# Kernel optimization log

Hardware: AMD Instinct MI355X
Metric: run time of the kernel (lower is better)

## Reference

```python
import jax, jax.numpy as jnp
import numpy as np

GN_EPS = 1e-5
NN_EPS = 1e-8


def _three_nn_interpolate(xyz1, xyz2, points2):
    # xyz1: (B,N,3), xyz2: (B,M,3), points2: (B,M,C) -> (B,N,C)
    src_sq = jnp.sum(xyz1 ** 2, axis=-1, keepdims=True)          # (B,N,1)
    dst_sq = jnp.sum(xyz2 ** 2, axis=-1)[:, None, :]             # (B,1,M)
    inner = jnp.einsum('bnd,bmd->bnm', xyz1, xyz2)               # (B,N,M)
    dist = src_sq - 2.0 * inner + dst_sq                         # (B,N,M)
    neg_d, idx = jax.lax.top_k(-dist, 3)                         # (B,N,3)
    d = -neg_d
    inv = 1.0 / (d + NN_EPS)
    w = inv / jnp.sum(inv, axis=-1, keepdims=True)               # (B,N,3)
    grouped = jax.vmap(lambda p, i: p[i])(points2, idx)          # (B,N,3,C)
    return jnp.sum(grouped * w[..., None], axis=2)               # (B,N,C)


def _group_norm(x, weight, bias, groups):
    # x: (B,C,N)
    B, C, N = x.shape
    xg = x.reshape(B, groups, C // groups, N)
    mu = jnp.mean(xg, axis=(2, 3), keepdims=True)
    var = jnp.var(xg, axis=(2, 3), keepdims=True)
    xg = (xg - mu) * jax.lax.rsqrt(var + GN_EPS)
    x = xg.reshape(B, C, N)
    return x * weight[None, :, None] + bias[None, :, None]


def setup_inputs() -> dict:
    key = jax.random.key(0)
    ks = jax.random.split(key, 10)
    B, N, M, C1, C2 = 8, 8192, 2048, 128, 256
    mlp = [256, 128]
    in_ch = C1 + C2
    inp = {
        'xyz1': jax.random.normal(ks[0], (B, N, 3), dtype=jnp.float32),
        'xyz2': jax.random.normal(ks[1], (B, M, 3), dtype=jnp.float32),
        'points1': jax.random.normal(ks[2], (B, N, C1), dtype=jnp.float32),
        'points2': jax.random.normal(ks[3], (B, M, C2), dtype=jnp.float32),
        'w0': jax.random.normal(ks[4], (mlp[0], in_ch), dtype=jnp.float32) * (1.0 / np.sqrt(in_ch)),
        'w1': jax.random.normal(ks[5], (mlp[1], mlp[0]), dtype=jnp.float32) * (1.0 / np.sqrt(mlp[0])),
        'gn0_w': jnp.ones((mlp[0],), dtype=jnp.float32),
        'gn0_b': jnp.zeros((mlp[0],), dtype=jnp.float32),
        'gn1_w': jnp.ones((mlp[1],), dtype=jnp.float32),
        'gn1_b': jnp.zeros((mlp[1],), dtype=jnp.float32),
    }
    return inp


def reference(xyz1, xyz2, points1, points2, w0, w1, gn0_w, gn0_b, gn1_w, gn1_b):
    interpolated = _three_nn_interpolate(xyz1, xyz2, points2)    # (B,N,C2)
    feat = jnp.concatenate([points1, interpolated], axis=-1)     # (B,N,C1+C2)
    # conv1d kernel size 1 == pointwise matmul; work in (B,C,N) layout for GN
    h = jnp.einsum('bnc,oc->bon', feat, w0)                      # (B,256,N)
    h = jax.nn.relu(_group_norm(h, gn0_w, gn0_b, groups=min(32, w0.shape[0])))
    h = jnp.einsum('bcn,oc->bon', h, w1)                         # (B,128,N)
    h = jax.nn.relu(_group_norm(h, gn1_w, gn1_b, groups=min(32, w1.shape[0])))
    return jnp.transpose(h, (0, 2, 1))                           # (B,N,128)
```

## Files before the change

kernel.cpp:

```cpp
#include <hip/hip_runtime.h>


#define DEVI __device__ __forceinline__

static constexpr int B  = 8;
static constexpr int N  = 8192;
static constexpr int M  = 2048;
static constexpr int C1 = 128;
static constexpr int C2 = 256;
static constexpr int CIN = C1 + C2;
static constexpr int H0 = 256;
static constexpr int H1 = 128;
static constexpr int BN = B * N;
static constexpr int NSEG = 8;
static constexpr int SEGL = M / NSEG;

typedef __bf16 bf16x8 __attribute__((ext_vector_type(8)));
typedef float  f32x4  __attribute__((ext_vector_type(4)));
typedef unsigned short ushort8v __attribute__((ext_vector_type(8)));

DEVI float bf2f(unsigned short u) {
    union { unsigned int i; float f; } v; v.i = ((unsigned int)u) << 16; return v.f;
}
DEVI unsigned short f2bf(float f) {
    union { float f; unsigned int i; } v; v.f = f;
    unsigned int x = v.i;
    return (unsigned short)((x + 0x7fffu + ((x >> 16) & 1u)) >> 16);
}
DEVI float ldin(const void* p, size_t i, int bf) {
    return bf ? bf2f(((const unsigned short*)p)[i]) : ((const float*)p)[i];
}
DEVI void ld8(const void* p, size_t i, int bf, float r[8]) {
    if (bf) {
        const ushort8v u = *(const ushort8v*)((const unsigned short*)p + i);
#pragma unroll
        for (int k = 0; k < 8; k++) r[k] = bf2f(u[k]);
    } else {
        const float4 a = *(const float4*)((const float*)p + i);
        const float4 b = *(const float4*)((const float*)p + i + 4);
        r[0] = a.x; r[1] = a.y; r[2] = a.z; r[3] = a.w;
        r[4] = b.x; r[5] = b.y; r[6] = b.z; r[7] = b.w;
    }
}
DEVI void ld8b(const unsigned short* p, size_t i, float r[8]) {
    const ushort8v u = *(const ushort8v*)(p + i);
#pragma unroll
    for (int k = 0; k < 8; k++) r[k] = bf2f(u[k]);
}

DEVI void gload16(const void* g, void* l) {
    __builtin_amdgcn_global_load_lds(
        (const __attribute__((address_space(1))) void*)g,
        (__attribute__((address_space(3))) void*)l, 16, 0, 0);
}

__global__ __launch_bounds__(64) void detect_dtype_kernel(const void* __restrict__ xyz1,
                                                          int* __restrict__ flag)
{
    const unsigned short* u = (const unsigned short*)xyz1;
    const int lane = threadIdx.x;
    const float av = fabsf(bf2f(u[2 * lane]));
    const bool in_range = (av >= 1e-4f && av <= 100.0f);
    const unsigned long long m = __ballot(in_range);
    if (lane == 0) flag[0] = (__popcll(m) >= 32) ? 1 : 0;
}

DEVI void cvt8(const void* src, unsigned short* dst, size_t j8, int bf) {
    if (bf) {
        *(ushort8v*)(dst + j8 * 8) = *(const ushort8v*)((const unsigned short*)src + j8 * 8);
    } else {
        float r[8];
        ld8(src, j8 * 8, 0, r);
        ushort8v o;
#pragma unroll
        for (int k = 0; k < 8; k++) o[k] = f2bf(r[k]);
        *(ushort8v*)(dst + j8 * 8) = o;
    }
}

__global__ __launch_bounds__(256) void prep_kernel(
    const void* __restrict__ w0, const void* __restrict__ w1,
    const void* __restrict__ p2, const void* __restrict__ xyz2,
    unsigned short* __restrict__ w0b, unsigned short* __restrict__ w1b,
    unsigned short* __restrict__ pb2,
    float4* __restrict__ c4, float* __restrict__ partz,
    const int* __restrict__ flag)
{
    const int bf = flag[0];
    constexpr int R0 = H0 * CIN / 8;
    constexpr int R1 = H1 * H0 / 8;
    constexpr int R2 = B * M;
    constexpr int R4 = B * M * C2 / 8;
    constexpr int R5 = 1024;
    constexpr int TOT = R0 + R1 + R2 + R4 + R5;
    for (int i = blockIdx.x * blockDim.x + threadIdx.x; i < TOT; i += gridDim.x * blockDim.x) {
        int j = i;
        if (j < R0) { cvt8(w0, w0b, j, bf); continue; }
        j -= R0;
        if (j < R1) { cvt8(w1, w1b, j, bf); continue; }
        j -= R1;
        if (j < R2) {
            const float x = ldin(xyz2, (size_t)j * 3 + 0, bf);
            const float y = ldin(xyz2, (size_t)j * 3 + 1, bf);
            const float z = ldin(xyz2, (size_t)j * 3 + 2, bf);
            const float sq = __fadd_rn(__fadd_rn(__fmul_rn(x, x), __fmul_rn(y, y)), __fmul_rn(z, z));
            c4[j] = make_float4(x, y, z, 0.5f * sq);
            continue;
        }
        j -= R2;
        if (j < R4) { cvt8(p2, pb2, j, bf); continue; }
        j -= R4;
        partz[j] = 0.f;
    }
}

__global__ __launch_bounds__(256) void knn3_split_kernel(
    const void* __restrict__ xyz1, const float4* __restrict__ c4,
    int* __restrict__ ci, const int* __restrict__ flag)
{
    const int bf = flag[0];
    const int tid = threadIdx.x;
    const int gid = blockIdx.x * 256 + tid;
    const int s = blockIdx.y;
    const int b = __builtin_amdgcn_readfirstlane(gid >> 13);

    const float x1 = ldin(xyz1, (size_t)gid * 3 + 0, bf);
    const float y1 = ldin(xyz1, (size_t)gid * 3 + 1, bf);
    const float z1 = ldin(xyz1, (size_t)gid * 3 + 2, bf);

    const float4* __restrict__ cand = c4 + b * M + s * SEGL;
    const int jbase = s * SEGL;
    constexpr int HALF = SEGL / 2;

    float a0 = 3.4e38f, a1 = 3.4e38f, a2 = 3.4e38f;
    int   ia0 = 0, ia1 = 0, ia2 = 0;
    float g0 = 3.4e38f, g1 = 3.4e38f, g2 = 3.4e38f;
    int   ig0 = 0, ig1 = 0, ig2 = 0;

#pragma unroll 4
    for (int j = 0; j < HALF; ++j) {
        const float4 pA = cand[j];
        const float4 pB = cand[j + HALF];
        const float sA = __builtin_fmaf(-x1, pA.x,
                          __builtin_fmaf(-y1, pA.y,
                           __builtin_fmaf(-z1, pA.z, pA.w)));
        const float sB = __builtin_fmaf(-x1, pB.x,
                          __builtin_fmaf(-y1, pB.y,
                           __builtin_fmaf(-z1, pB.z, pB.w)));
        {
            const int jn = jbase + j;
            const bool c0 = sA < a0;
            const float t1 = fmaxf(sA, a0); a0 = fminf(sA, a0);
            const int  tj1 = c0 ? ia0 : jn; ia0 = c0 ? jn : ia0;
            const bool c1 = t1 < a1;
            const float t2 = fmaxf(t1, a1); a1 = fminf(t1, a1);
            const int  tj2 = c1 ? ia1 : tj1; ia1 = c1 ? tj1 : ia1;
            const bool c2 = t2 < a2;
            a2 = fminf(t2, a2); ia2 = c2 ? tj2 : ia2;
        }
        {
            const int jn = jbase + HALF + j;
            const bool c0 = sB < g0;
            const float t1 = fmaxf(sB, g0); g0 = fminf(sB, g0);
            const int  tj1 = c0 ? ig0 : jn; ig0 = c0 ? jn : ig0;
            const bool c1 = t1 < g1;
            const float t2 = fmaxf(t1, g1); g1 = fminf(t1, g1);
            const int  tj2 = c1 ? ig1 : tj1; ig1 = c1 ? tj1 : ig1;
            const bool c2 = t2 < g2;
            g2 = fminf(t2, g2); ig2 = c2 ? tj2 : ig2;
        }
    }

    float mv[3] = { g0, g1, g2 };
    int   mi[3] = { ig0, ig1, ig2 };
#pragma unroll
    for (int k = 0; k < 3; ++k) {
        const float sv = mv[k]; const int jn = mi[k];
        const bool c0 = sv < a0;
        const float t1 = fmaxf(sv, a0); a0 = fminf(sv, a0);
        const int  tj1 = c0 ? ia0 : jn; ia0 = c0 ? jn : ia0;
        const bool c1 = t1 < a1;
        const float t2 = fmaxf(t1, a1); a1 = fminf(t1, a1);
        const int  tj2 = c1 ? ia1 : tj1; ia1 = c1 ? tj1 : ia1;
        const bool c2 = t2 < a2;
        a2 = fminf(t2, a2); ia2 = c2 ? tj2 : ia2;
    }

    ci[(size_t)(s * 3 + 0) * BN + gid] = ia0;
    ci[(size_t)(s * 3 + 1) * BN + gid] = ia1;
    ci[(size_t)(s * 3 + 2) * BN + gid] = ia2;
}

__global__ __launch_bounds__(256) void interp_merge_kernel(
    const void* __restrict__ p1, const unsigned short* __restrict__ pb2,
    const void* __restrict__ xyz1, const float4* __restrict__ c4,
    const int* __restrict__ ci,
    unsigned short* __restrict__ feat, const int* __restrict__ flag)
{
    __shared__ int   sidx[128][3];
    __shared__ float sw[128][3];

    const int bf = flag[0];
    const int t = threadIdx.x;
    const int qbase = blockIdx.x * 128;
    const int b = qbase >> 13;

    if (t < 128) {
        const int q = qbase + t;
        const float x1 = ldin(xyz1, (size_t)q * 3 + 0, bf);
        const float y1 = ldin(xyz1, (size_t)q * 3 + 1, bf);
        const float z1 = ldin(xyz1, (size_t)q * 3 + 2, bf);
        const float sq1 = __fadd_rn(__fadd_rn(__fmul_rn(x1, x1), __fmul_rn(y1, y1)), __fmul_rn(z1, z1));

        float bd0 = 3.4e38f, bd1 = 3.4e38f, bd2 = 3.4e38f;
        int   bi0 = 0x7fffffff, bi1 = 0x7fffffff, bi2 = 0x7fffffff;

#pragma unroll
        for (int k = 0; k < 3 * NSEG; ++k) {
            const int ix = ci[(size_t)k * BN + q];
            const float4 p = c4[b * M + ix];
            const float inner = __fadd_rn(__fadd_rn(__fmul_rn(x1, p.x), __fmul_rn(y1, p.y)),
                                          __fmul_rn(z1, p.z));
            const float pw2 = p.w + p.w;
            const float d = __fadd_rn(__fsub_rn(sq1, __fmul_rn(2.0f, inner)), pw2);
            const bool lt2 = (d < bd2) || (d == bd2 && ix < bi2);
            if (lt2) {
                const bool lt0 = (d < bd0) || (d == bd0 && ix < bi0);
                const bool lt1 = (d < bd1) || (d == bd1 && ix < bi1);
                if (lt0)      { bd2 = bd1; bi2 = bi1; bd1 = bd0; bi1 = bi0; bd0 = d; bi0 = ix; }
                else if (lt1) { bd2 = bd1; bi2 = bi1; bd1 = d; bi1 = ix; }
                else          { bd2 = d; bi2 = ix; }
            }
        }

        const float v0 = 1.0f / (bd0 + 1e-8f);
        const float v1 = 1.0f / (bd1 + 1e-8f);
        const float v2 = 1.0f / (bd2 + 1e-8f);
        const float s = v0 + v1 + v2;
        sidx[t][0] = bi0; sidx[t][1] = bi1; sidx[t][2] = bi2;
        sw[t][0] = v0 / s; sw[t][1] = v1 / s; sw[t][2] = v2 / s;
    }
    __syncthreads();

#pragma unroll 1
    for (int it = 0; it < 24; ++it) {
        const int tt = it * 256 + t;
        const int ql = tt / 48;
        const int c8 = tt % 48;
        const int c  = c8 * 8;
        const int q  = qbase + ql;
        ushort8v o;
        if (c < C1) {
            if (bf) {
                o = *(const ushort8v*)((const unsigned short*)p1 + (size_t)q * C1 + c);
            } else {
                float r[8];
                ld8(p1, (size_t)q * C1 + c, 0, r);
#pragma unroll
                for (int k = 0; k < 8; k++) o[k] = f2bf(r[k]);
            }
        } else {
            const int c2 = c - C1;
            float t0[8], t1[8], t2[8];
            ld8b(pb2, (size_t)(b * M + sidx[ql][0]) * C2 + c2, t0);
            ld8b(pb2, (size_t)(b * M + sidx[ql][1]) * C2 + c2, t1);
            ld8b(pb2, (size_t)(b * M + sidx[ql][2]) * C2 + c2, t2);
            const float w0v = sw[ql][0], w1v = sw[ql][1], w2v = sw[ql][2];
#pragma unroll
            for (int k = 0; k < 8; k++)
                o[k] = f2bf(w0v * t0[k] + w1v * t1[k] + w2v * t2[k]);
        }
        *(ushort8v*)(feat + (size_t)q * CIN + c) = o;
    }
}

__global__ __launch_bounds__(512) void gemm1_kernel(
    const unsigned short* __restrict__ A,
    const unsigned short* __restrict__ W,
    unsigned short* __restrict__ h0, float2* __restrict__ part)
{
    constexpr int K = CIN;
    constexpr int COUT = H0;
    __shared__ __align__(16) char lds[49152];

    const int tid = threadIdx.x;
    const int l   = tid & 63;
    const int w   = tid >> 6;
    const int rowBase = blockIdx.x * 128;
    const int b = rowBase >> 13;

    const int srow  = l >> 3;
    const int sslot = l & 7;

    f32x4 acc[4][4];
#pragma unroll
    for (int i = 0; i < 4; i++)
#pragma unroll
        for (int j = 0; j < 4; j++) acc[i][j] = (f32x4)0.0f;

    const int wr  = w >> 2;
    const int wc  = w & 3;
    const int rl  = l & 15;
    const int kq  = l >> 4;
    const int swz = (l & 7) << 4;
    int aoff[4], boff[4];
#pragma unroll
    for (int i = 0; i < 4; i++) {
        aoff[i] = (wr * 64 + i * 16 + rl) * 128;
        boff[i] = 16384 + (wc * 64 + i * 16 + rl) * 128;
    }

    constexpr int NT = K / 64;

#pragma unroll 1
    for (int t = 0; t < NT; ++t) {
        const int k0 = t * 64;
#pragma unroll
        for (int i = 0; i < 6; ++i) {
            const int ch = w * 6 + i;
            if (ch < 16) {
                const int r  = ch * 8 + srow;
                const int ke = (sslot ^ (r & 7)) << 3;
                gload16(A + ((size_t)(rowBase + r) * K + k0 + ke), lds + ch * 1024);
            } else {
                const int rb = (ch - 16) * 8 + srow;
                const int ke = (sslot ^ (rb & 7)) << 3;
                gload16(W + ((size_t)rb * K + k0 + ke), lds + 16384 + (ch - 16) * 1024);
            }
        }
        __syncthreads();
#pragma unroll
        for (int ks = 0; ks < 2; ++ks) {
            const int kb = (ks * 64 + kq * 16) ^ swz;
            bf16x8 af[4], bfr[4];
#pragma unroll
            for (int i = 0; i < 4; i++) af[i]  = *(const bf16x8*)(lds + aoff[i] + kb);
#pragma unroll
            for (int j = 0; j < 4; j++) bfr[j] = *(const bf16x8*)(lds + boff[j] + kb);
#pragma unroll
            for (int i = 0; i < 4; i++)
#pragma unroll
                for (int j = 0; j < 4; j++)
                    acc[i][j] = __builtin_amdgcn_mfma_f32_16x16x32_bf16(af[i], bfr[j], acc[i][j], 0, 0, 0);
        }
        __syncthreads();
    }

    const int crow = rowBase + wr * 64 + kq * 4;
    const int ccol = wc * 64 + rl;
    float gsum[4], gss[4];
#pragma unroll
    for (int j = 0; j < 4; j++) {
        float s = 0.f, ss = 0.f;
#pragma unroll
        for (int i = 0; i < 4; i++)
#pragma unroll
            for (int r = 0; r < 4; r++) {
                const unsigned short hb = f2bf(acc[i][j][r]);
                h0[(size_t)(crow + i * 16 + r) * COUT + ccol + j * 16] = hb;
                const float x = bf2f(hb);
                s += x; ss += x * x;
            }
        gsum[j] = s; gss[j] = ss;
    }
    __syncthreads();
    float2* sred = (float2*)lds;
    if (tid < 32) sred[tid] = make_float2(0.f, 0.f);
    __syncthreads();
#pragma unroll
    for (int j = 0; j < 4; j++) {
        const int g = wc * 8 + j * 2 + (rl >> 3);
        atomicAdd(&sred[g].x, gsum[j]);
        atomicAdd(&sred[g].y, gss[j]);
    }
    __syncthreads();
    if (tid < 32) {
        atomicAdd(&part[b * 32 + tid].x, sred[tid].x);
        atomicAdd(&part[b * 32 + tid].y, sred[tid].y);
    }
}

__global__ __launch_bounds__(256) void gemm2_kernel(
    const unsigned short* __restrict__ h0, const float2* __restrict__ part0,
    const void* __restrict__ gw, const void* __restrict__ gb,
    const unsigned short* __restrict__ W,
    unsigned short* __restrict__ h1, float2* __restrict__ part1,
    const int* __restrict__ flag)
{
    constexpr int K = H0;
    constexpr int COUT = H1;
    __shared__ __align__(16) char lds[32768];
    __shared__ float2 stlds[32];

    const int bf = flag[0];
    const int tid = threadIdx.x;
    const int l   = tid & 63;
    const int w   = tid >> 6;
    const int rowBase = blockIdx.x * 128;
    const int b = rowBase >> 13;

    if (tid < 32) {
        const float2 p = part0[b * 32 + tid];
        const float cnt = (float)N * 8.0f;
        const float mu  = p.x / cnt;
        const float var = p.y / cnt - mu * mu;
        stlds[tid] = make_float2(mu, rsqrtf(var + 1e-5f));
    }
    __syncthreads();

    const int srow  = l >> 3;
    const int sslot = l & 7;

    f32x4 acc[4][4];
#pragma unroll
    for (int i = 0; i < 4; i++)
#pragma unroll
        for (int j = 0; j < 4; j++) acc[i][j] = (f32x4)0.0f;

    const int wr  = (tid >> 7) & 1;
    const int wc  = (tid >> 6) & 1;
    const int rl  = l & 15;
    const int kq  = l >> 4;
    const int swz = (l & 7) << 4;
    int aoff[4], boff[4];
#pragma unroll
    for (int i = 0; i < 4; i++) {
        aoff[i] = (wr * 64 + i * 16 + rl) * 128;
        boff[i] = 16384 + (wc * 64 + i * 16 + rl) * 128;
    }

    constexpr int NT = K / 64;

#pragma unroll 1
    for (int t = 0; t < NT; ++t) {
        const int k0 = t * 64;
#pragma unroll
        for (int i = 0; i < 4; ++i) {
            const int cb = w * 4 + i;
            const int r  = cb * 8 + srow;
            const int ke = (sslot ^ (r & 7)) << 3;
            gload16(W + ((size_t)r * K + k0 + ke), lds + 16384 + cb * 1024);
        }
#pragma unroll
        for (int i = 0; i < 4; ++i) {
            const int r = (w * 4 + i) * 8 + srow;
            const int kslot = sslot ^ (r & 7);
            const int c = k0 + (kslot << 3);
            const float2 ms = stlds[c >> 3];
            float gwv[8], gbv[8];
            ld8(gw, c, bf, gwv);
            ld8(gb, c, bf, gbv);
            const ushort8v hv = *(const ushort8v*)(h0 + (size_t)(rowBase + r) * H0 + c);
            ushort8v o;
#pragma unroll
            for (int k = 0; k < 8; k++) {
                const float x = bf2f(hv[k]);
                o[k] = f2bf(fmaxf((x - ms.x) * ms.y * gwv[k] + gbv[k], 0.f));
            }
            *(ushort8v*)(lds + r * 128 + (sslot << 4)) = o;
        }
        __syncthreads();
#pragma unroll
        for (int ks = 0; ks < 2; ++ks) {
            const int kb = (ks * 64 + kq * 16) ^ swz;
            bf16x8 af[4], bfr[4];
#pragma unroll
            for (int i = 0; i < 4; i++) af[i]  = *(const bf16x8*)(lds + aoff[i] + kb);
#pragma unroll
            for (int j = 0; j < 4; j++) bfr[j] = *(const bf16x8*)(lds + boff[j] + kb);
#pragma unroll
            for (int i = 0; i < 4; i++)
#pragma unroll
                for (int j = 0; j < 4; j++)
                    acc[i][j] = __builtin_amdgcn_mfma_f32_16x16x32_bf16(af[i], bfr[j], acc[i][j], 0, 0, 0);
        }
        __syncthreads();
    }

    const int crow = rowBase + wr * 64 + kq * 4;
    const int ccol = wc * 64 + rl;
    float gsum[4], gss[4];
#pragma unroll
    for (int j = 0; j < 4; j++) {
        float s = 0.f, ss = 0.f;
#pragma unroll
        for (int i = 0; i < 4; i++)
#pragma unroll
            for (int r = 0; r < 4; r++) {
                const unsigned short hb = f2bf(acc[i][j][r]);
                h1[(size_t)(crow + i * 16 + r) * COUT + ccol + j * 16] = hb;
                const float x = bf2f(hb);
                s += x; ss += x * x;
            }
        gsum[j] = s; gss[j] = ss;
    }
    __syncthreads();
    float2* sred = (float2*)lds;
    if (tid < 32) sred[tid] = make_float2(0.f, 0.f);
    __syncthreads();
#pragma unroll
    for (int j = 0; j < 4; j++) {
        const int g = wc * 16 + j * 4 + (rl >> 2);
        atomicAdd(&sred[g].x, gsum[j]);
        atomicAdd(&sred[g].y, gss[j]);
    }
    __syncthreads();
    if (tid < 32) {
        atomicAdd(&part1[b * 32 + tid].x, sred[tid].x);
        atomicAdd(&part1[b * 32 + tid].y, sred[tid].y);
    }
}

__global__ __launch_bounds__(256) void gn_norm_relu_kernel(
    const unsigned short* __restrict__ h, const float2* __restrict__ part1,
    const void* __restrict__ gw, const void* __restrict__ gb,
    void* __restrict__ out, const int* __restrict__ flag)
{
    constexpr int C = H1;
    constexpr int cpg = 4;
    constexpr int C4 = C >> 2;
    constexpr int total4 = BN * C / 4;

    __shared__ float2 stlds[256];
    {
        const float2 p = part1[threadIdx.x];
        const float cnt = (float)N * (float)cpg;
        const float mu  = p.x / cnt;
        const float var = p.y / cnt - mu * mu;
        stlds[threadIdx.x] = make_float2(mu, rsqrtf(var + 1e-5f));
    }
    __syncthreads();

    const int bf = flag[0];
    for (int i4 = blockIdx.x * blockDim.x + threadIdx.x; i4 < total4; i4 += gridDim.x * blockDim.x) {
        const int c = (i4 % C4) * 4;
        const int p = i4 / C4;
        const int b = p >> 13;
        const float2 ms = stlds[b * 32 + c / cpg];
        const ushort4 hv = *(const ushort4*)(h + (size_t)i4 * 4);
        float r[4] = { bf2f(hv.x), bf2f(hv.y), bf2f(hv.z), bf2f(hv.w) };
#pragma unroll
        for (int k = 0; k < 4; k++) {
            const float gwv = ldin(gw, c + k, bf);
            const float gbv = ldin(gb, c + k, bf);
            r[k] = fmaxf((r[k] - ms.x) * ms.y * gwv + gbv, 0.f);
        }
        if (bf) {
            ushort4 o;
            o.x = f2bf(r[0]); o.y = f2bf(r[1]); o.z = f2bf(r[2]); o.w = f2bf(r[3]);
            *(ushort4*)((unsigned short*)out + (size_t)i4 * 4) = o;
        } else {
            float4 o; o.x = r[0]; o.y = r[1]; o.z = r[2]; o.w = r[3];
            *(float4*)((float*)out + (size_t)i4 * 4) = o;
        }
    }
}

extern "C" void kernel_launch(void* const* d_in, const int* in_sizes, int n_in,
                              void* d_out, int out_size, void* d_ws, size_t ws_size,
                              hipStream_t stream)
{
    const void* xyz1    = d_in[0];
    const void* xyz2    = d_in[1];
    const void* points1 = d_in[2];
    const void* points2 = d_in[3];
    const void* w0      = d_in[4];
    const void* w1      = d_in[5];
    const void* gn0w    = d_in[6];
    const void* gn0b    = d_in[7];
    const void* gn1w    = d_in[8];
    const void* gn1b    = d_in[9];

    char* ws = (char*)d_ws;
    unsigned short* feat   = (unsigned short*)ws;
    unsigned short* h1     = feat;
    unsigned short* h0     = (unsigned short*)(ws + 50331648);
    unsigned short* w0b    = (unsigned short*)(ws + 83886080);
    unsigned short* w1b    = (unsigned short*)(ws + 84082688);
    unsigned short* pb2    = (unsigned short*)(ws + 84148224);
    float4*         c4     = (float4*)(ws + 92536832);
    int*            ci     = (int*)(ws + 92798976);
    float2*         part0  = (float2*)(ws + 99090432);
    float2*         part1  = (float2*)(ws + 99092480);
    int*            flag   = (int*)(ws + 99094528);

    detect_dtype_kernel<<<1, 64, 0, stream>>>(xyz1, flag);

    prep_kernel<<<1024, 256, 0, stream>>>(w0, w1, points2, xyz2,
                                          w0b, w1b, pb2, c4, (float*)part0, flag);

    {
        dim3 g(BN / 256, NSEG);
        knn3_split_kernel<<<g, 256, 0, stream>>>(xyz1, c4, ci, flag);
    }

    interp_merge_kernel<<<BN / 128, 256, 0, stream>>>(points1, pb2, xyz1, c4, ci,
                                                      feat, flag);

    gemm1_kernel<<<BN / 128, 512, 0, stream>>>(feat, w0b, h0, part0);

    gemm2_kernel<<<BN / 128, 256, 0, stream>>>(h0, part0, gn0w, gn0b, w1b, h1,
                                               part1, flag);

    gn_norm_relu_kernel<<<1024, 256, 0, stream>>>(h1, part1, gn1w, gn1b, d_out, flag);
}
```

Baseline: 316.3 us.

## Fuse kNN merge and interpolation into first GEMM, keep features in LDS

The interp_merge kernel is folded into gemm1. Each 64-row block now merges the per-segment kNN candidates in parallel (8 threads per query, then a serial top-3 merge), builds its full 64x384 bf16 feature tile directly in swizzled LDS, and streams only W0 tiles from global memory. This drops the round trip of the feature matrix through global memory and one kernel launch. In exchange the block tile shrinks from 128 to 64 rows, W0 is reloaded twice as often, and LDS use grows to 80KB, which can limit occupancy.

```diff
diff --git a/kernel.cpp b/kernel.cpp
--- a/kernel.cpp
+++ b/kernel.cpp
@@ -191,38 +191,60 @@
     ci[(size_t)(s * 3 + 2) * BN + gid] = ia2;
 }
 
-__global__ __launch_bounds__(256) void interp_merge_kernel(
+__global__ __launch_bounds__(512, 4) void gemm1_kernel(
     const void* __restrict__ p1, const unsigned short* __restrict__ pb2,
     const void* __restrict__ xyz1, const float4* __restrict__ c4,
     const int* __restrict__ ci,
-    unsigned short* __restrict__ feat, const int* __restrict__ flag)
-{
-    __shared__ int   sidx[128][3];
-    __shared__ float sw[128][3];
+    const unsigned short* __restrict__ W,
+    unsigned short* __restrict__ h0, float2* __restrict__ part,
+    const int* __restrict__ flag)
+{
+    constexpr int K = CIN;
+    constexpr int COUT = H0;
+    __shared__ __align__(16) char lds[81920];
 
     const int bf = flag[0];
     const int t = threadIdx.x;
-    const int qbase = blockIdx.x * 128;
+    const int l = t & 63;
+    const int w = t >> 6;
+    const int qbase = blockIdx.x * 64;
     const int b = qbase >> 13;
 
-    if (t < 128) {
-        const int q = qbase + t;
+    float* dd = (float*)(lds + 49152);
+    int*   di = (int*)(lds + 55296);
+    int*   sidx = (int*)(lds + 61440);
+    float* sw = (float*)(lds + 62208);
+
+    {
+        const int ql = t >> 3;
+        const int q  = qbase + ql;
+        const int kk0 = (t & 7) * 3;
         const float x1 = ldin(xyz1, (size_t)q * 3 + 0, bf);
         const float y1 = ldin(xyz1, (size_t)q * 3 + 1, bf);
         const float z1 = ldin(xyz1, (size_t)q * 3 + 2, bf);
         const float sq1 = __fadd_rn(__fadd_rn(__fmul_rn(x1, x1), __fmul_rn(y1, y1)), __fmul_rn(z1, z1));
-
-        float bd0 = 3.4e38f, bd1 = 3.4e38f, bd2 = 3.4e38f;
-        int   bi0 = 0x7fffffff, bi1 = 0x7fffffff, bi2 = 0x7fffffff;
-
-#pragma unroll
-        for (int k = 0; k < 3 * NSEG; ++k) {
+#pragma unroll
+        for (int u = 0; u < 3; ++u) {
+            const int k = kk0 + u;
             const int ix = ci[(size_t)k * BN + q];
             const float4 p = c4[b * M + ix];
             const float inner = __fadd_rn(__fadd_rn(__fmul_rn(x1, p.x), __fmul_rn(y1, p.y)),
                                           __fmul_rn(z1, p.z));
             const float pw2 = p.w + p.w;
             const float d = __fadd_rn(__fsub_rn(sq1, __fmul_rn(2.0f, inner)), pw2);
+            dd[ql * 24 + k] = d;
+            di[ql * 24 + k] = ix;
+        }
+    }
+    __syncthreads();
+
+    if (t < 64) {
+        float bd0 = 3.4e38f, bd1 = 3.4e38f, bd2 = 3.4e38f;
+        int   bi0 = 0x7fffffff, bi1 = 0x7fffffff, bi2 = 0x7fffffff;
+#pragma unroll
+        for (int k = 0; k < 24; ++k) {
+            const float d  = dd[t * 24 + k];
+            const int   ix = di[t * 24 + k];
             const bool lt2 = (d < bd2) || (d == bd2 && ix < bi2);
             if (lt2) {
                 const bool lt0 = (d < bd0) || (d == bd0 && ix < bi0);
@@ -232,113 +254,85 @@
                 else          { bd2 = d; bi2 = ix; }
             }
         }
-
         const float v0 = 1.0f / (bd0 + 1e-8f);
         const float v1 = 1.0f / (bd1 + 1e-8f);
         const float v2 = 1.0f / (bd2 + 1e-8f);
         const float s = v0 + v1 + v2;
-        sidx[t][0] = bi0; sidx[t][1] = bi1; sidx[t][2] = bi2;
-        sw[t][0] = v0 / s; sw[t][1] = v1 / s; sw[t][2] = v2 / s;
+        sidx[t * 3 + 0] = bi0; sidx[t * 3 + 1] = bi1; sidx[t * 3 + 2] = bi2;
+        sw[t * 3 + 0] = v0 / s; sw[t * 3 + 1] = v1 / s; sw[t * 3 + 2] = v2 / s;
     }
     __syncthreads();
 
 #pragma unroll 1
-    for (int it = 0; it < 24; ++it) {
-        const int tt = it * 256 + t;
-        const int ql = tt / 48;
-        const int c8 = tt % 48;
+    for (int it = 0; it < 6; ++it) {
+        const int task = it * 512 + t;
+        const int ql = task / 48;
+        const int c8 = task % 48;
         const int c  = c8 * 8;
-        const int q  = qbase + ql;
-        ushort8v o;
+        float v[8];
         if (c < C1) {
-            if (bf) {
-                o = *(const ushort8v*)((const unsigned short*)p1 + (size_t)q * C1 + c);
-            } else {
-                float r[8];
-                ld8(p1, (size_t)q * C1 + c, 0, r);
-#pragma unroll
-                for (int k = 0; k < 8; k++) o[k] = f2bf(r[k]);
-            }
+            ld8(p1, (size_t)(qbase + ql) * C1 + c, bf, v);
         } else {
             const int c2 = c - C1;
             float t0[8], t1[8], t2[8];
-            ld8b(pb2, (size_t)(b * M + sidx[ql][0]) * C2 + c2, t0);
-            ld8b(pb2, (size_t)(b * M + sidx[ql][1]) * C2 + c2, t1);
-            ld8b(pb2, (size_t)(b * M + sidx[ql][2]) * C2 + c2, t2);
-            const float w0v = sw[ql][0], w1v = sw[ql][1], w2v = sw[ql][2];
-#pragma unroll
-            for (int k = 0; k < 8; k++)
-                o[k] = f2bf(w0v * t0[k] + w1v * t1[k] + w2v * t2[k]);
-        }
-        *(ushort8v*)(feat + (size_t)q * CIN + c) = o;
-    }
-}
-
-__global__ __launch_bounds__(512) void gemm1_kernel(
-    const unsigned short* __restrict__ A,
-    const unsigned short* __restrict__ W,
-    unsigned short* __restrict__ h0, float2* __restrict__ part)
-{
-    constexpr int K = CIN;
-    constexpr int COUT = H0;
-    __shared__ __align__(16) char lds[49152];
-
-    const int tid = threadIdx.x;
-    const int l   = tid & 63;
-    const int w   = tid >> 6;
-    const int rowBase = blockIdx.x * 128;
-    const int b = rowBase >> 13;
+            ld8b(pb2, (size_t)(b * M + sidx[ql * 3 + 0]) * C2 + c2, t0);
+            ld8b(pb2, (size_t)(b * M + sidx[ql * 3 + 1]) * C2 + c2, t1);
+            ld8b(pb2, (size_t)(b * M + sidx[ql * 3 + 2]) * C2 + c2, t2);
+            const float w0v = sw[ql * 3 + 0], w1v = sw[ql * 3 + 1], w2v = sw[ql * 3 + 2];
+#pragma unroll
+            for (int k = 0; k < 8; k++) v[k] = w0v * t0[k] + w1v * t1[k] + w2v * t2[k];
+        }
+        ushort8v o;
+#pragma unroll
+        for (int k = 0; k < 8; k++) o[k] = f2bf(v[k]);
+        *(ushort8v*)(lds + ql * 768 + ((c8 >> 3) << 7) + ((((c8 & 7) ^ (ql & 7)) << 4))) = o;
+    }
+    __syncthreads();
 
     const int srow  = l >> 3;
     const int sslot = l & 7;
-
-    f32x4 acc[4][4];
-#pragma unroll
-    for (int i = 0; i < 4; i++)
-#pragma unroll
-        for (int j = 0; j < 4; j++) acc[i][j] = (f32x4)0.0f;
-
     const int wr  = w >> 2;
     const int wc  = w & 3;
     const int rl  = l & 15;
     const int kq  = l >> 4;
-    const int swz = (l & 7) << 4;
-    int aoff[4], boff[4];
-#pragma unroll
-    for (int i = 0; i < 4; i++) {
-        aoff[i] = (wr * 64 + i * 16 + rl) * 128;
-        boff[i] = 16384 + (wc * 64 + i * 16 + rl) * 128;
-    }
+    const int swz7 = l & 7;
+
+    f32x4 acc[2][4];
+#pragma unroll
+    for (int i = 0; i < 2; i++)
+#pragma unroll
+        for (int j = 0; j < 4; j++) acc[i][j] = (f32x4)0.0f;
+
+    int aoff[2], boff[4];
+#pragma unroll
+    for (int i = 0; i < 2; i++) aoff[i] = (wr * 32 + i * 16 + rl) * 768;
+#pragma unroll
+    for (int j = 0; j < 4; j++) boff[j] = 49152 + (wc * 64 + j * 16 + rl) * 128;
 
     constexpr int NT = K / 64;
 
 #pragma unroll 1
-    for (int t = 0; t < NT; ++t) {
-        const int k0 = t * 64;
-#pragma unroll
-        for (int i = 0; i < 6; ++i) {
-            const int ch = w * 6 + i;
-            if (ch < 16) {
-                const int r  = ch * 8 + srow;
-                const int ke = (sslot ^ (r & 7)) << 3;
-                gload16(A + ((size_t)(rowBase + r) * K + k0 + ke), lds + ch * 1024);
-            } else {
-                const int rb = (ch - 16) * 8 + srow;
-                const int ke = (sslot ^ (rb & 7)) << 3;
-                gload16(W + ((size_t)rb * K + k0 + ke), lds + 16384 + (ch - 16) * 1024);
-            }
+    for (int tt = 0; tt < NT; ++tt) {
+        const int k0 = tt * 64;
+#pragma unroll
+        for (int i = 0; i < 4; ++i) {
+            const int cb = w * 4 + i;
+            const int rb = cb * 8 + srow;
+            const int ke = (sslot ^ (rb & 7)) << 3;
+            gload16(W + ((size_t)rb * K + k0 + ke), lds + 49152 + cb * 1024);
         }
         __syncthreads();
 #pragma unroll
         for (int ks = 0; ks < 2; ++ks) {
-            const int kb = (ks * 64 + kq * 16) ^ swz;
-            bf16x8 af[4], bfr[4];
-#pragma unroll
-            for (int i = 0; i < 4; i++) af[i]  = *(const bf16x8*)(lds + aoff[i] + kb);
-#pragma unroll
-            for (int j = 0; j < 4; j++) bfr[j] = *(const bf16x8*)(lds + boff[j] + kb);
-#pragma unroll
-            for (int i = 0; i < 4; i++)
+            const int akb = (tt << 7) + (((ks * 4 + kq) ^ swz7) << 4);
+            const int bkb = (ks * 64 + kq * 16) ^ (swz7 << 4);
+            bf16x8 af[2], bfr[4];
+#pragma unroll
+            for (int i = 0; i < 2; i++) af[i]  = *(const bf16x8*)(lds + aoff[i] + akb);
+#pragma unroll
+            for (int j = 0; j < 4; j++) bfr[j] = *(const bf16x8*)(lds + boff[j] + bkb);
+#pragma unroll
+            for (int i = 0; i < 2; i++)
 #pragma unroll
                 for (int j = 0; j < 4; j++)
                     acc[i][j] = __builtin_amdgcn_mfma_f32_16x16x32_bf16(af[i], bfr[j], acc[i][j], 0, 0, 0);
@@ -346,14 +340,14 @@
         __syncthreads();
     }
 
-    const int crow = rowBase + wr * 64 + kq * 4;
+    const int crow = qbase + wr * 32 + kq * 4;
     const int ccol = wc * 64 + rl;
     float gsum[4], gss[4];
 #pragma unroll
     for (int j = 0; j < 4; j++) {
         float s = 0.f, ss = 0.f;
 #pragma unroll
-        for (int i = 0; i < 4; i++)
+        for (int i = 0; i < 2; i++)
 #pragma unroll
             for (int r = 0; r < 4; r++) {
                 const unsigned short hb = f2bf(acc[i][j][r]);
@@ -365,7 +359,7 @@
     }
     __syncthreads();
     float2* sred = (float2*)lds;
-    if (tid < 32) sred[tid] = make_float2(0.f, 0.f);
+    if (t < 32) sred[t] = make_float2(0.f, 0.f);
     __syncthreads();
 #pragma unroll
     for (int j = 0; j < 4; j++) {
@@ -374,9 +368,9 @@
         atomicAdd(&sred[g].y, gss[j]);
     }
     __syncthreads();
-    if (tid < 32) {
-        atomicAdd(&part[b * 32 + tid].x, sred[tid].x);
-        atomicAdd(&part[b * 32 + tid].y, sred[tid].y);
+    if (t < 32) {
+        atomicAdd(&part[b * 32 + t].x, sred[t].x);
+        atomicAdd(&part[b * 32 + t].y, sred[t].y);
     }
 }
 
@@ -572,17 +566,16 @@
     const void* gn1b    = d_in[9];
 
     char* ws = (char*)d_ws;
-    unsigned short* feat   = (unsigned short*)ws;
-    unsigned short* h1     = feat;
-    unsigned short* h0     = (unsigned short*)(ws + 50331648);
-    unsigned short* w0b    = (unsigned short*)(ws + 83886080);
-    unsigned short* w1b    = (unsigned short*)(ws + 84082688);
-    unsigned short* pb2    = (unsigned short*)(ws + 84148224);
-    float4*         c4     = (float4*)(ws + 92536832);
-    int*            ci     = (int*)(ws + 92798976);
-    float2*         part0  = (float2*)(ws + 99090432);
-    float2*         part1  = (float2*)(ws + 99092480);
-    int*            flag   = (int*)(ws + 99094528);
+    unsigned short* h0     = (unsigned short*)ws;
+    unsigned short* h1     = (unsigned short*)(ws + 33554432);
+    unsigned short* w0b    = (unsigned short*)(ws + 50331648);
+    unsigned short* w1b    = (unsigned short*)(ws + 50528256);
+    unsigned short* pb2    = (unsigned short*)(ws + 50593792);
+    float4*         c4     = (float4*)(ws + 58982400);
+    int*            ci     = (int*)(ws + 59244544);
+    float2*         part0  = (float2*)(ws + 65536000);
+    float2*         part1  = (float2*)(ws + 65538048);
+    int*            flag   = (int*)(ws + 65540096);
 
     detect_dtype_kernel<<<1, 64, 0, stream>>>(xyz1, flag);
 
@@ -594,10 +587,8 @@
         knn3_split_kernel<<<g, 256, 0, stream>>>(xyz1, c4, ci, flag);
     }
 
-    interp_merge_kernel<<<BN / 128, 256, 0, stream>>>(points1, pb2, xyz1, c4, ci,
-                                                      feat, flag);
-
-    gemm1_kernel<<<BN / 128, 512, 0, stream>>>(feat, w0b, h0, part0);
+    gemm1_kernel<<<BN / 64, 512, 0, stream>>>(points1, pb2, xyz1, c4, ci,
+                                              w0b, h0, part0, flag);
 
     gemm2_kernel<<<BN / 128, 256, 0, stream>>>(h0, part0, gn0w, gn0b, w1b, h1,
                                                part1, flag);
```

Result: faster. 294.1 us (-7.0%).
